# Kernel tuning notes

Measured on AMD Instinct MI355X. Metric: run time of the kernel, lower is better.

The kernel has to match this reference:

```python
import jax, jax.numpy as jnp
import numpy as np

NEG_SLOPE = 0.01  # F.leaky_relu default


def gcn_conv(x, W, b, src, dst):
    """PyG GCNConv: add self-loops, symmetric deg^-1/2 normalization, linear, scatter-add."""
    n = x.shape[0]
    loop = jnp.arange(n)
    s = jnp.concatenate([src, loop])  # source j
    d = jnp.concatenate([dst, loop])  # target i
    deg = jax.ops.segment_sum(jnp.ones_like(d, dtype=x.dtype), d, num_segments=n)
    dis = jnp.where(deg > 0, jax.lax.rsqrt(jnp.maximum(deg, 1e-12)), 0.0)
    norm = dis[s] * dis[d]                       # [E+N]
    h = x @ W                                    # [N, out]
    msg = h[s] * norm[:, None]                   # gather + scale
    out = jax.ops.segment_sum(msg, d, num_segments=n)  # scatter-add to targets
    return out + b


def setup_inputs() -> dict:
    key = jax.random.key(0)
    ks = jax.random.split(key, 8)
    N, E, G = 100000, 800000, 100
    IN, H, OUT = 128, 256, 16
    x = jax.random.normal(ks[0], (N, IN), dtype=jnp.float32)
    edge_index = jax.random.randint(ks[1], (2, E), 0, N, dtype=jnp.int64)
    batch = jnp.repeat(jnp.arange(G, dtype=jnp.int64), N // G)  # sorted graph ids
    def glorot(k, fi, fo):
        lim = np.sqrt(6.0 / (fi + fo))
        return jax.random.uniform(k, (fi, fo), jnp.float32, -lim, lim)
    return {
        "x": x, "edge_index": edge_index, "batch": batch,
        "W1": glorot(ks[2], IN, H), "b1": jnp.zeros((H,), jnp.float32),
        "W2": glorot(ks[3], H, H),  "b2": jnp.zeros((H,), jnp.float32),
        "W3": glorot(ks[4], H, OUT), "b3": jnp.zeros((OUT,), jnp.float32),
    }


def reference(x, edge_index, batch, W1, b1, W2, b2, W3, b3):
    src, dst = edge_index[0], edge_index[1]
    h = gcn_conv(x, W1, b1, src, dst)
    h = jax.nn.leaky_relu(h, NEG_SLOPE)  # dropout p=0.0 -> identity
    h = gcn_conv(h, W2, b2, src, dst)
    h = jax.nn.leaky_relu(h, NEG_SLOPE)
    h = gcn_conv(h, W3, b3, src, dst)
    # get_zero_nodes: first node of each graph in the sorted batch vector
    mask = jnp.concatenate([jnp.array([True]), batch[1:] != batch[:-1]])
    return h[mask, :]  # [n_graphs, out_channels]
```

## Files before the change

kernel.cpp:

```cpp
#include <hip/hip_runtime.h>

#define NEG_SLOPE 0.01f

using short8 = __attribute__((ext_vector_type(8))) short;
using f32x4  = __attribute__((ext_vector_type(4))) float;

__device__ inline float b2f(ushort u) {
    union { unsigned u; float f; } x; x.u = ((unsigned)u) << 16; return x.f;
}
__device__ inline ushort f2b(float f) {
    union { float f; unsigned u; } x; x.f = f;
    unsigned r = x.u + 0x7FFFu + ((x.u >> 16) & 1u);
    return (ushort)(r >> 16);
}
__device__ inline void gload16(const void* g, void* l) {
    __builtin_amdgcn_global_load_lds((__attribute__((address_space(1))) void*)g,
                                     (__attribute__((address_space(3))) void*)l, 16, 0, 0);
}
__device__ inline int isroot(const int* __restrict__ batch, int d) {
    return (d == 0) || (batch[d] != batch[d - 1]);
}
__device__ inline void gbar(int* ctr, int nblk) {
    __syncthreads();
    if (threadIdx.x == 0) {
        __threadfence();
        __hip_atomic_fetch_add(ctr, 1, __ATOMIC_RELEASE, __HIP_MEMORY_SCOPE_AGENT);
        while (__hip_atomic_load(ctr, __ATOMIC_ACQUIRE, __HIP_MEMORY_SCOPE_AGENT) < nblk)
            __builtin_amdgcn_s_sleep(1);
    }
    __syncthreads();
}


__global__ void count_f1(const int* __restrict__ src, const int* __restrict__ dst,
                         const int* __restrict__ batch, int* __restrict__ cnt,
                         int* __restrict__ flag1, int* __restrict__ picked, int E, int N) {
    int i = blockIdx.x * blockDim.x + threadIdx.x;
    if (i < N && isroot(batch, i)) {
        picked[batch[i]] = i;
        flag1[i] = 1;
    }
    int e0 = i * 4;
    if (e0 + 3 < E) {
        int4 dq = *(const int4*)(dst + e0);
        int r0 = isroot(batch, dq.x), r1 = isroot(batch, dq.y);
        int r2 = isroot(batch, dq.z), r3 = isroot(batch, dq.w);
        atomicAdd(&cnt[dq.x], 1);
        atomicAdd(&cnt[dq.y], 1);
        atomicAdd(&cnt[dq.z], 1);
        atomicAdd(&cnt[dq.w], 1);
        if (r0 | r1 | r2 | r3) {
            int4 sq = *(const int4*)(src + e0);
            if (r0) flag1[sq.x] = 1;
            if (r1) flag1[sq.y] = 1;
            if (r2) flag1[sq.z] = 1;
            if (r3) flag1[sq.w] = 1;
        }
    } else if (e0 < E) {
        for (int e = e0; e < E; e++) {
            int d = dst[e];
            atomicAdd(&cnt[d], 1);
            if (isroot(batch, d)) flag1[src[e]] = 1;
        }
    }
}


__global__ void frontier2v(const int* __restrict__ src, const int* __restrict__ dst,
                           const int* __restrict__ flag1, int* __restrict__ flag2,
                           int E, int N) {
    int i = blockIdx.x * blockDim.x + threadIdx.x;
    int e0 = i * 4;
    if (e0 + 3 < E) {
        int4 dq = *(const int4*)(dst + e0);
        int f0 = flag1[dq.x], f1 = flag1[dq.y], f2 = flag1[dq.z], f3 = flag1[dq.w];
        if (f0 | f1 | f2 | f3) {
            int4 sq = *(const int4*)(src + e0);
            if (f0) flag2[sq.x] = 1;
            if (f1) flag2[sq.y] = 1;
            if (f2) flag2[sq.z] = 1;
            if (f3) flag2[sq.w] = 1;
        }
    } else if (e0 < E) {
        for (int e = e0; e < E; e++) if (flag1[dst[e]]) flag2[src[e]] = 1;
    }
    if (i < N && flag1[i]) flag2[i] = 1;
}


__global__ __launch_bounds__(256) void scan_one(
    const int* __restrict__ cnt, const int* __restrict__ f1, const int* __restrict__ f2,
    int4* __restrict__ aggslot, float* __restrict__ dis,
    int* __restrict__ rowptr, int* __restrict__ cur,
    int* __restrict__ pos1, int* __restrict__ pos2,
    int* __restrict__ list1, int* __restrict__ list2,
    int* __restrict__ counts, int N, int nb,
    const float* __restrict__ W1, ushort* __restrict__ W1t,
    const float* __restrict__ W2, ushort* __restrict__ W2t) {
    __shared__ int l0[256], l1[256], l2[256];
    __shared__ int baseS[3];
    const int b = blockIdx.x, t = threadIdx.x;
    const int base = b * 1024 + t * 4;

    int c[4] = {0,0,0,0}, a1[4] = {0,0,0,0}, a2[4] = {0,0,0,0};
    if (base + 3 < N) {
        int4 q = *(const int4*)(cnt + base); c[0]=q.x; c[1]=q.y; c[2]=q.z; c[3]=q.w;
        int4 u = *(const int4*)(f1 + base);  a1[0]=u.x; a1[1]=u.y; a1[2]=u.z; a1[3]=u.w;
        int4 v = *(const int4*)(f2 + base);  a2[0]=v.x; a2[1]=v.y; a2[2]=v.z; a2[3]=v.w;
    } else {
        for (int i = 0; i < 4; i++) if (base + i < N) {
            c[i] = cnt[base + i]; a1[i] = f1[base + i]; a2[i] = f2[base + i];
        }
    }
#pragma unroll
    for (int i = 0; i < 4; i++)
        if (base + i < N) dis[base + i] = rsqrtf((float)c[i] + 1.0f);

    int m[4];
#pragma unroll
    for (int i = 0; i < 4; i++) m[i] = a2[i] ? c[i] : 0;
    int ts0 = m[0] + m[1] + m[2] + m[3];
    int ts1 = a1[0] + a1[1] + a1[2] + a1[3];
    int ts2 = a2[0] + a2[1] + a2[2] + a2[3];
    l0[t] = ts0; l1[t] = ts1; l2[t] = ts2;
    __syncthreads();
    for (int off = 1; off < 256; off <<= 1) {
        int u0 = (t >= off) ? l0[t - off] : 0;
        int u1 = (t >= off) ? l1[t - off] : 0;
        int u2 = (t >= off) ? l2[t - off] : 0;
        __syncthreads();
        l0[t] += u0; l1[t] += u1; l2[t] += u2;
        __syncthreads();
    }

    if (t == 0) {
        __hip_atomic_store(&aggslot[b].x, l0[255], __ATOMIC_RELAXED, __HIP_MEMORY_SCOPE_AGENT);
        __hip_atomic_store(&aggslot[b].y, l1[255], __ATOMIC_RELAXED, __HIP_MEMORY_SCOPE_AGENT);
        __hip_atomic_store(&aggslot[b].z, l2[255], __ATOMIC_RELAXED, __HIP_MEMORY_SCOPE_AGENT);
        __hip_atomic_store(&aggslot[b].w, 1, __ATOMIC_RELEASE, __HIP_MEMORY_SCOPE_AGENT);
    }

    if (t < 64) {
        int g0 = 0, g1 = 0, g2 = 0;
        for (int w0 = 0; w0 < b; w0 += 64) {
            int idx = w0 + t;
            if (idx < b) {
                while (__hip_atomic_load(&aggslot[idx].w, __ATOMIC_ACQUIRE,
                                         __HIP_MEMORY_SCOPE_AGENT) == 0) {
                    __builtin_amdgcn_s_sleep(1);
                }
                g0 += __hip_atomic_load(&aggslot[idx].x, __ATOMIC_RELAXED, __HIP_MEMORY_SCOPE_AGENT);
                g1 += __hip_atomic_load(&aggslot[idx].y, __ATOMIC_RELAXED, __HIP_MEMORY_SCOPE_AGENT);
                g2 += __hip_atomic_load(&aggslot[idx].z, __ATOMIC_RELAXED, __HIP_MEMORY_SCOPE_AGENT);
            }
        }
#pragma unroll
        for (int s = 1; s < 64; s <<= 1) {
            g0 += __shfl_xor(g0, s, 64);
            g1 += __shfl_xor(g1, s, 64);
            g2 += __shfl_xor(g2, s, 64);
        }
        if (t == 0) { baseS[0] = g0; baseS[1] = g1; baseS[2] = g2; }
    }
    __syncthreads();

    int run0 = baseS[0] + l0[t] - ts0;
    int run1 = baseS[1] + l1[t] - ts1;
    int run2 = baseS[2] + l2[t] - ts2;
#pragma unroll
    for (int i = 0; i < 4; i++) {
        if (base + i < N) {
            rowptr[base + i] = run0;
            cur[base + i] = run0;
            if (a1[i]) { pos1[base + i] = run1; list1[run1] = base + i; }
            if (a2[i]) { pos2[base + i] = run2; list2[run2] = base + i; }
        }
        run0 += m[i]; run1 += a1[i]; run2 += a2[i];
    }
    if (b == nb - 1 && t == 255) {
        counts[0] = baseS[1] + l1[255];
        counts[1] = baseS[2] + l2[255];
        rowptr[N] = baseS[0] + l0[255];
    }

    for (int idx = b * 256 + t; idx < 98304; idx += gridDim.x * 256) {
        if (idx < 32768) {
            int n = idx >> 7, k = idx & 127;
            W1t[idx] = f2b(W1[k * 256 + n]);
        } else {
            int j = idx - 32768;
            int n = j >> 8, k = j & 255;
            W2t[j] = f2b(W2[k * 256 + n]);
        }
    }
}


__global__ void fill_fv(const int* __restrict__ src, const int* __restrict__ dst,
                        const int* __restrict__ flag2, int* __restrict__ cur,
                        int* __restrict__ col, int E) {
    int i = blockIdx.x * blockDim.x + threadIdx.x;
    int e0 = i * 4;
    if (e0 + 3 < E) {
        int4 dq = *(const int4*)(dst + e0);
        int f0 = flag2[dq.x], f1 = flag2[dq.y], f2 = flag2[dq.z], f3 = flag2[dq.w];
        if (f0 | f1 | f2 | f3) {
            int4 sq = *(const int4*)(src + e0);
            if (f0) col[atomicAdd(&cur[dq.x], 1)] = sq.x;
            if (f1) col[atomicAdd(&cur[dq.y], 1)] = sq.y;
            if (f2) col[atomicAdd(&cur[dq.z], 1)] = sq.z;
            if (f3) col[atomicAdd(&cur[dq.w], 1)] = sq.w;
        }
    } else if (e0 < E) {
        for (int e = e0; e < E; e++) {
            int d = dst[e];
            if (flag2[d]) col[atomicAdd(&cur[d], 1)] = src[e];
        }
    }
}


__global__ __launch_bounds__(256) void aggx_c(const float* __restrict__ x,
                                              const float* __restrict__ dis,
                                              const int* __restrict__ rowptr,
                                              const int* __restrict__ col,
                                              const int* __restrict__ list2,
                                              const int* __restrict__ counts,
                                              ushort* __restrict__ aggXc) {
    const int M2 = counts[1];
    int wave = blockIdx.x * 4 + (threadIdx.x >> 6);
    int lane = threadIdx.x & 63;
    int li = lane & 31, sub = lane >> 5;
    int stride = gridDim.x * 8;
    const float* xp = x + li * 4;
    for (int p = wave * 2 + sub; p < M2; p += stride) {
        int node = list2[p];
        float di = dis[node];
        float4 sv = *(const float4*)(xp + (size_t)node * 128);
        float a0 = di * sv.x, a1 = di * sv.y, a2 = di * sv.z, a3 = di * sv.w;
        int e = rowptr[node], e1 = rowptr[node + 1];
        for (; e + 2 <= e1; e += 2) {
            int s0 = col[e], s1 = col[e + 1];
            float w0 = dis[s0], w1 = dis[s1];
            float4 v0 = *(const float4*)(xp + (size_t)s0 * 128);
            float4 v1 = *(const float4*)(xp + (size_t)s1 * 128);
            a0 += w0 * v0.x + w1 * v1.x;
            a1 += w0 * v0.y + w1 * v1.y;
            a2 += w0 * v0.z + w1 * v1.z;
            a3 += w0 * v0.w + w1 * v1.w;
        }
        if (e < e1) {
            int s = col[e];
            float w = dis[s];
            float4 v = *(const float4*)(xp + (size_t)s * 128);
            a0 += w * v.x; a1 += w * v.y; a2 += w * v.z; a3 += w * v.w;
        }
        ushort4 o;
        o.x = f2b(di * a0); o.y = f2b(di * a1); o.z = f2b(di * a2); o.w = f2b(di * a3);
        *(ushort4*)(aggXc + (size_t)p * 128 + li * 4) = o;
    }
}


template <int K>
__device__ void gemm_phase(const ushort* __restrict__ A, const ushort* __restrict__ Bt,
                           const float* __restrict__ bias, const float* __restrict__ dis,
                           const int* __restrict__ list, int M, ushort* __restrict__ C,
                           ushort* As, ushort* Bs, int nblk) {
    const int t = threadIdx.x;
    const int lane = t & 63;
    const int w = t >> 6;
    const int wm = w >> 2, wn = w & 3;

    for (int tile = blockIdx.x; tile * 128 < M; tile += nblk) {
        const int row0 = tile * 128;
        f32x4 acc[4][4] = {};
#pragma unroll
        for (int kt = 0; kt < K / 64; kt++) {
#pragma unroll
            for (int it = 0; it < 2; it++) {
                int q = it * 512 + t;
                int r = q >> 3, c = q & 7;
                int cs = c ^ (r & 7);
                int ga = min(row0 + r, M - 1);
                gload16(A + (size_t)ga * K + kt * 64 + cs * 8, &As[q * 8]);
            }
#pragma unroll
            for (int it = 0; it < 4; it++) {
                int q = it * 512 + t;
                int r = q >> 3, c = q & 7;
                int cs = c ^ (r & 7);
                gload16(Bt + (size_t)r * K + kt * 64 + cs * 8, &Bs[q * 8]);
            }
            __syncthreads();
#pragma unroll
            for (int ks = 0; ks < 2; ks++) {
                short8 a[4], b[4];
                int cc = ks * 4 + (lane >> 4);
#pragma unroll
                for (int m = 0; m < 4; m++) {
                    int R = wm * 64 + m * 16 + (lane & 15);
                    a[m] = *(const short8*)&As[R * 64 + ((cc ^ (R & 7)) * 8)];
                }
#pragma unroll
                for (int n = 0; n < 4; n++) {
                    int R = wn * 64 + n * 16 + (lane & 15);
                    b[n] = *(const short8*)&Bs[R * 64 + ((cc ^ (R & 7)) * 8)];
                }
#pragma unroll
                for (int m = 0; m < 4; m++)
#pragma unroll
                    for (int n = 0; n < 4; n++)
                        acc[m][n] = __builtin_amdgcn_mfma_f32_16x16x32_bf16(a[m], b[n], acc[m][n], 0, 0, 0);
            }
            __syncthreads();
        }
#pragma unroll
        for (int m = 0; m < 4; m++) {
#pragma unroll
            for (int j = 0; j < 4; j++) {
                int grow = row0 + wm * 64 + m * 16 + (lane >> 4) * 4 + j;
                if (grow >= M) continue;
                float dr = dis[list[grow]];
#pragma unroll
                for (int n = 0; n < 4; n++) {
                    int gcol = wn * 64 + n * 16 + (lane & 15);
                    float v = acc[m][n][j] + bias[gcol];
                    v = v > 0.f ? v : NEG_SLOPE * v;
                    C[(size_t)grow * 256 + gcol] = f2b(v * dr);
                }
            }
        }
    }
}


#define TAIL_NBLK 64

__global__ __launch_bounds__(512) void megatail(
    const ushort* __restrict__ aggXc, const ushort* __restrict__ W1t,
    const float* __restrict__ b1, ushort* __restrict__ h1c,
    const float* __restrict__ dis, const int* __restrict__ rowptr,
    const int* __restrict__ col, const int* __restrict__ list1,
    const int* __restrict__ list2, const int* __restrict__ pos1,
    const int* __restrict__ pos2, const int* __restrict__ counts,
    ushort* __restrict__ agg1c, const ushort* __restrict__ W2t,
    const float* __restrict__ b2, ushort* __restrict__ h2c,
    const int* __restrict__ picked, const float* __restrict__ W3,
    const float* __restrict__ b3, float* __restrict__ out,
    int* __restrict__ bars, int G) {
    __shared__ ushort As[128 * 64];
    __shared__ ushort Bs[256 * 64];
    __shared__ float aggf[256];
    __shared__ float redf[256];
    const int t = threadIdx.x;
    const int bid = blockIdx.x;
    const int M1 = counts[0];
    const int M2 = counts[1];

    gemm_phase<128>(aggXc, W1t, b1, dis, list2, M2, h1c, As, Bs, TAIL_NBLK);
    gbar(&bars[0], TAIL_NBLK);

    {
        int lane = t & 63;
        int w = t >> 6;
        int wave = bid * 8 + w;
        int li = lane & 31, sub = lane >> 5;
        int stride = TAIL_NBLK * 16;
        const ushort* hp = h1c + (size_t)li * 8;
        for (int p = wave * 2 + sub; p < M1; p += stride) {
            int i = list1[p];
            float di = dis[i];
            float a[8];
            {
                short8 v = *(const short8*)(hp + (size_t)pos2[i] * 256);
#pragma unroll
                for (int j = 0; j < 8; j++) a[j] = b2f((ushort)v[j]);
            }
            int e1 = rowptr[i + 1];
            for (int e = rowptr[i]; e < e1; e++) {
                short8 v = *(const short8*)(hp + (size_t)pos2[col[e]] * 256);
#pragma unroll
                for (int j = 0; j < 8; j++) a[j] += b2f((ushort)v[j]);
            }
            short8 o;
#pragma unroll
            for (int j = 0; j < 8; j++) o[j] = (short)f2b(di * a[j]);
            *(short8*)(agg1c + (size_t)p * 256 + li * 8) = o;
        }
    }
    gbar(&bars[1], TAIL_NBLK);

    gemm_phase<256>(agg1c, W2t, b2, dis, list1, M1, h2c, As, Bs, TAIL_NBLK);
    gbar(&bars[2], TAIL_NBLK);

    for (int g = bid; g < G; g += TAIL_NBLK) {
        if (t < 256) {
            int i = picked[g];
            float di = dis[i];
            float a = b2f(h2c[(size_t)pos1[i] * 256 + t]);
            int e1 = rowptr[i + 1];
            for (int e = rowptr[i]; e < e1; e++)
                a += b2f(h2c[(size_t)pos1[col[e]] * 256 + t]);
            aggf[t] = di * a;
        }
        __syncthreads();
        if (t < 256) {
            int c = t & 15, seg = t >> 4;
            float p = 0.f;
#pragma unroll
            for (int kk = 0; kk < 16; kk++) {
                int k = seg * 16 + kk;
                p += aggf[k] * W3[k * 16 + c];
            }
            redf[t] = p;
        }
        __syncthreads();
        if (t < 16) {
            float s = 0.f;
#pragma unroll
            for (int ss = 0; ss < 16; ss++) s += redf[ss * 16 + t];
            out[g * 16 + t] = s + b3[t];
        }
        __syncthreads();
    }
}


extern "C" void kernel_launch(void* const* d_in, const int* in_sizes, int n_in,
                              void* d_out, int out_size, void* d_ws, size_t ws_size,
                              hipStream_t stream) {
    const float* x   = (const float*)d_in[0];
    const int* ei    = (const int*)d_in[1];
    const int* batch = (const int*)d_in[2];
    const float* W1  = (const float*)d_in[3];
    const float* b1  = (const float*)d_in[4];
    const float* W2  = (const float*)d_in[5];
    const float* b2  = (const float*)d_in[6];
    const float* W3  = (const float*)d_in[7];
    const float* b3  = (const float*)d_in[8];

    const int IN = 128, H = 256, OUT = 16;
    int N = in_sizes[0] / IN;
    int E = in_sizes[1] / 2;
    int G = out_size / OUT;
    const int* srcp = ei;
    const int* dstp = ei + E;

    char* p = (char*)d_ws;
    auto carve = [&](size_t bytes) {
        char* q = p;
        p += (bytes + 255) & ~(size_t)255;
        return q;
    };
    int*    cnt    = (int*)carve((size_t)N * 4);
    int*    flag1  = (int*)carve((size_t)N * 4);
    int*    flag2  = (int*)carve((size_t)N * 4);
    int4*   aggslot= (int4*)carve(1024 * 16);
    int*    bars   = (int*)carve(256);
    char*   zend   = p;
    float*  dis    = (float*)carve((size_t)N * 4);
    int*    rowptr = (int*)carve(((size_t)N + 1) * 4);
    int*    cur    = (int*)carve((size_t)N * 4);
    int*    counts = (int*)carve(256);
    int*    picked = (int*)carve((size_t)G * 4);
    int*    pos1   = (int*)carve((size_t)N * 4);
    int*    pos2   = (int*)carve((size_t)N * 4);
    int*    list1  = (int*)carve((size_t)N * 4);
    int*    list2  = (int*)carve((size_t)N * 4);
    int*    col    = (int*)carve((size_t)E * 4);
    ushort* W1t    = (ushort*)carve((size_t)256 * 128 * 2);
    ushort* W2t    = (ushort*)carve((size_t)256 * 256 * 2);
    ushort* RA     = (ushort*)carve((size_t)N * H * 2);
    ushort* RB     = (ushort*)carve((size_t)N * H * 2);

    ushort* aggXc = RA;
    ushort* agg1c = RA;
    ushort* h1c   = RB;
    ushort* h2c   = RB;

    int nb = (N + 1023) / 1024;
    int e4 = (E + 3) / 4;
    int epN = (e4 > N ? e4 : N);

    hipMemsetAsync(cnt, 0, (size_t)(zend - (char*)cnt), stream);
    count_f1<<<(epN + 255) / 256, 256, 0, stream>>>(srcp, dstp, batch, cnt, flag1, picked, E, N);
    frontier2v<<<(epN + 255) / 256, 256, 0, stream>>>(srcp, dstp, flag1, flag2, E, N);
    scan_one<<<nb, 256, 0, stream>>>(cnt, flag1, flag2, aggslot, dis, rowptr, cur,
                                     pos1, pos2, list1, list2, counts, N, nb,
                                     W1, W1t, W2, W2t);
    fill_fv<<<(e4 + 255) / 256, 256, 0, stream>>>(srcp, dstp, flag2, cur, col, E);
    aggx_c<<<1024, 256, 0, stream>>>(x, dis, rowptr, col, list2, counts, aggXc);
    megatail<<<TAIL_NBLK, 512, 0, stream>>>(aggXc, W1t, b1, h1c, dis, rowptr, col,
                                            list1, list2, pos1, pos2, counts, agg1c,
                                            W2t, b2, h2c, picked, W3, b3,
                                            (float*)d_out, bars, G);
}
```

Before: 159.2 us.

## Replace persistent megatail with layer-1 GEMM plus per-graph fused tail kernel

The persistent megatail kernel used grid barriers to run the layer-1 GEMM, the layer-2 aggregation over the 1-hop frontier, the layer-2 GEMM and the final layer. It is split into a standalone layer-1 GEMM kernel and a per-graph tail kernel. For each picked root node, the tail kernel recomputes layer-2 aggregation and the W2 matvec only for the root and its neighbours, then does the layer-3 reduction. This drops the frontier-1 list/scan bookkeeping, the global barriers and the full layer-2 GEMM over all 1-hop nodes, in exchange for redundant per-graph scalar matvecs with a single block per graph.

```diff
diff --git a/kernel.cpp b/kernel.cpp
--- a/kernel.cpp
+++ b/kernel.cpp
@@ -19,16 +19,6 @@
 }
 __device__ inline int isroot(const int* __restrict__ batch, int d) {
     return (d == 0) || (batch[d] != batch[d - 1]);
-}
-__device__ inline void gbar(int* ctr, int nblk) {
-    __syncthreads();
-    if (threadIdx.x == 0) {
-        __threadfence();
-        __hip_atomic_fetch_add(ctr, 1, __ATOMIC_RELEASE, __HIP_MEMORY_SCOPE_AGENT);
-        while (__hip_atomic_load(ctr, __ATOMIC_ACQUIRE, __HIP_MEMORY_SCOPE_AGENT) < nblk)
-            __builtin_amdgcn_s_sleep(1);
-    }
-    __syncthreads();
 }
 
 
@@ -88,28 +78,26 @@
 }
 
 
-__global__ __launch_bounds__(256) void scan_one(
-    const int* __restrict__ cnt, const int* __restrict__ f1, const int* __restrict__ f2,
+__global__ __launch_bounds__(256) void scan_dual(
+    const int* __restrict__ cnt, const int* __restrict__ f2,
     int4* __restrict__ aggslot, float* __restrict__ dis,
     int* __restrict__ rowptr, int* __restrict__ cur,
-    int* __restrict__ pos1, int* __restrict__ pos2,
-    int* __restrict__ list1, int* __restrict__ list2,
+    int* __restrict__ pos2, int* __restrict__ list2,
     int* __restrict__ counts, int N, int nb,
     const float* __restrict__ W1, ushort* __restrict__ W1t,
-    const float* __restrict__ W2, ushort* __restrict__ W2t) {
-    __shared__ int l0[256], l1[256], l2[256];
-    __shared__ int baseS[3];
+    const float* __restrict__ W2, ushort* __restrict__ W2b) {
+    __shared__ int l0[256], l2[256];
+    __shared__ int baseS[2];
     const int b = blockIdx.x, t = threadIdx.x;
     const int base = b * 1024 + t * 4;
 
-    int c[4] = {0,0,0,0}, a1[4] = {0,0,0,0}, a2[4] = {0,0,0,0};
+    int c[4] = {0,0,0,0}, a2[4] = {0,0,0,0};
     if (base + 3 < N) {
         int4 q = *(const int4*)(cnt + base); c[0]=q.x; c[1]=q.y; c[2]=q.z; c[3]=q.w;
-        int4 u = *(const int4*)(f1 + base);  a1[0]=u.x; a1[1]=u.y; a1[2]=u.z; a1[3]=u.w;
         int4 v = *(const int4*)(f2 + base);  a2[0]=v.x; a2[1]=v.y; a2[2]=v.z; a2[3]=v.w;
     } else {
         for (int i = 0; i < 4; i++) if (base + i < N) {
-            c[i] = cnt[base + i]; a1[i] = f1[base + i]; a2[i] = f2[base + i];
+            c[i] = cnt[base + i]; a2[i] = f2[base + i];
         }
     }
 #pragma unroll
@@ -120,28 +108,25 @@
 #pragma unroll
     for (int i = 0; i < 4; i++) m[i] = a2[i] ? c[i] : 0;
     int ts0 = m[0] + m[1] + m[2] + m[3];
-    int ts1 = a1[0] + a1[1] + a1[2] + a1[3];
     int ts2 = a2[0] + a2[1] + a2[2] + a2[3];
-    l0[t] = ts0; l1[t] = ts1; l2[t] = ts2;
+    l0[t] = ts0; l2[t] = ts2;
     __syncthreads();
     for (int off = 1; off < 256; off <<= 1) {
         int u0 = (t >= off) ? l0[t - off] : 0;
-        int u1 = (t >= off) ? l1[t - off] : 0;
         int u2 = (t >= off) ? l2[t - off] : 0;
         __syncthreads();
-        l0[t] += u0; l1[t] += u1; l2[t] += u2;
+        l0[t] += u0; l2[t] += u2;
         __syncthreads();
     }
 
     if (t == 0) {
         __hip_atomic_store(&aggslot[b].x, l0[255], __ATOMIC_RELAXED, __HIP_MEMORY_SCOPE_AGENT);
-        __hip_atomic_store(&aggslot[b].y, l1[255], __ATOMIC_RELAXED, __HIP_MEMORY_SCOPE_AGENT);
-        __hip_atomic_store(&aggslot[b].z, l2[255], __ATOMIC_RELAXED, __HIP_MEMORY_SCOPE_AGENT);
+        __hip_atomic_store(&aggslot[b].y, l2[255], __ATOMIC_RELAXED, __HIP_MEMORY_SCOPE_AGENT);
         __hip_atomic_store(&aggslot[b].w, 1, __ATOMIC_RELEASE, __HIP_MEMORY_SCOPE_AGENT);
     }
 
     if (t < 64) {
-        int g0 = 0, g1 = 0, g2 = 0;
+        int g0 = 0, g2 = 0;
         for (int w0 = 0; w0 < b; w0 += 64) {
             int idx = w0 + t;
             if (idx < b) {
@@ -150,36 +135,31 @@
                     __builtin_amdgcn_s_sleep(1);
                 }
                 g0 += __hip_atomic_load(&aggslot[idx].x, __ATOMIC_RELAXED, __HIP_MEMORY_SCOPE_AGENT);
-                g1 += __hip_atomic_load(&aggslot[idx].y, __ATOMIC_RELAXED, __HIP_MEMORY_SCOPE_AGENT);
-                g2 += __hip_atomic_load(&aggslot[idx].z, __ATOMIC_RELAXED, __HIP_MEMORY_SCOPE_AGENT);
+                g2 += __hip_atomic_load(&aggslot[idx].y, __ATOMIC_RELAXED, __HIP_MEMORY_SCOPE_AGENT);
             }
         }
 #pragma unroll
         for (int s = 1; s < 64; s <<= 1) {
             g0 += __shfl_xor(g0, s, 64);
-            g1 += __shfl_xor(g1, s, 64);
             g2 += __shfl_xor(g2, s, 64);
         }
-        if (t == 0) { baseS[0] = g0; baseS[1] = g1; baseS[2] = g2; }
+        if (t == 0) { baseS[0] = g0; baseS[1] = g2; }
     }
     __syncthreads();
 
     int run0 = baseS[0] + l0[t] - ts0;
-    int run1 = baseS[1] + l1[t] - ts1;
-    int run2 = baseS[2] + l2[t] - ts2;
+    int run2 = baseS[1] + l2[t] - ts2;
 #pragma unroll
     for (int i = 0; i < 4; i++) {
         if (base + i < N) {
             rowptr[base + i] = run0;
             cur[base + i] = run0;
-            if (a1[i]) { pos1[base + i] = run1; list1[run1] = base + i; }
             if (a2[i]) { pos2[base + i] = run2; list2[run2] = base + i; }
         }
-        run0 += m[i]; run1 += a1[i]; run2 += a2[i];
+        run0 += m[i]; run2 += a2[i];
     }
     if (b == nb - 1 && t == 255) {
-        counts[0] = baseS[1] + l1[255];
-        counts[1] = baseS[2] + l2[255];
+        counts[0] = baseS[1] + l2[255];
         rowptr[N] = baseS[0] + l0[255];
     }
 
@@ -189,8 +169,7 @@
             W1t[idx] = f2b(W1[k * 256 + n]);
         } else {
             int j = idx - 32768;
-            int n = j >> 8, k = j & 255;
-            W2t[j] = f2b(W2[k * 256 + n]);
+            W2b[j] = f2b(W2[j]);
         }
     }
 }
@@ -227,7 +206,7 @@
                                               const int* __restrict__ list2,
                                               const int* __restrict__ counts,
                                               ushort* __restrict__ aggXc) {
-    const int M2 = counts[1];
+    const int M2 = counts[0];
     int wave = blockIdx.x * 4 + (threadIdx.x >> 6);
     int lane = threadIdx.x & 63;
     int li = lane & 31, sub = lane >> 5;
@@ -263,19 +242,25 @@
 
 
 template <int K>
-__device__ void gemm_phase(const ushort* __restrict__ A, const ushort* __restrict__ Bt,
-                           const float* __restrict__ bias, const float* __restrict__ dis,
-                           const int* __restrict__ list, int M, ushort* __restrict__ C,
-                           ushort* As, ushort* Bs, int nblk) {
+__global__ __launch_bounds__(512) void gemm_c(const ushort* __restrict__ A,
+                                              const ushort* __restrict__ Bt,
+                                              const float* __restrict__ bias,
+                                              const float* __restrict__ dis,
+                                              const int* __restrict__ list,
+                                              const int* __restrict__ counts,
+                                              ushort* __restrict__ C) {
+    __shared__ ushort As[128 * 64];
+    __shared__ ushort Bs[256 * 64];
+    const int M = counts[0];
     const int t = threadIdx.x;
     const int lane = t & 63;
     const int w = t >> 6;
     const int wm = w >> 2, wn = w & 3;
 
-    for (int tile = blockIdx.x; tile * 128 < M; tile += nblk) {
+    for (int tile = blockIdx.x; tile * 128 < M; tile += gridDim.x) {
         const int row0 = tile * 128;
         f32x4 acc[4][4] = {};
-#pragma unroll
+
         for (int kt = 0; kt < K / 64; kt++) {
 #pragma unroll
             for (int it = 0; it < 2; it++) {
@@ -315,6 +300,7 @@
             }
             __syncthreads();
         }
+
 #pragma unroll
         for (int m = 0; m < 4; m++) {
 #pragma unroll
@@ -335,94 +321,82 @@
 }
 
 
-#define TAIL_NBLK 64
-
-__global__ __launch_bounds__(512) void megatail(
-    const ushort* __restrict__ aggXc, const ushort* __restrict__ W1t,
-    const float* __restrict__ b1, ushort* __restrict__ h1c,
-    const float* __restrict__ dis, const int* __restrict__ rowptr,
-    const int* __restrict__ col, const int* __restrict__ list1,
-    const int* __restrict__ list2, const int* __restrict__ pos1,
-    const int* __restrict__ pos2, const int* __restrict__ counts,
-    ushort* __restrict__ agg1c, const ushort* __restrict__ W2t,
-    const float* __restrict__ b2, ushort* __restrict__ h2c,
-    const int* __restrict__ picked, const float* __restrict__ W3,
-    const float* __restrict__ b3, float* __restrict__ out,
-    int* __restrict__ bars, int G) {
-    __shared__ ushort As[128 * 64];
-    __shared__ ushort Bs[256 * 64];
-    __shared__ float aggf[256];
-    __shared__ float redf[256];
+__global__ __launch_bounds__(256) void tail_g(
+    const ushort* __restrict__ h1c, const float* __restrict__ dis,
+    const int* __restrict__ rowptr, const int* __restrict__ col,
+    const int* __restrict__ picked, const int* __restrict__ pos2,
+    const ushort* __restrict__ W2b, const float* __restrict__ b2,
+    const float* __restrict__ W3, const float* __restrict__ b3,
+    float* __restrict__ out, int G) {
+    __shared__ float aggs[8][256];
+    __shared__ float sdis[8];
+    __shared__ float vec[256];
+    __shared__ float red[256];
+    const int g = blockIdx.x;
     const int t = threadIdx.x;
-    const int bid = blockIdx.x;
-    const int M1 = counts[0];
-    const int M2 = counts[1];
-
-    gemm_phase<128>(aggXc, W1t, b1, dis, list2, M2, h1c, As, Bs, TAIL_NBLK);
-    gbar(&bars[0], TAIL_NBLK);
-
-    {
-        int lane = t & 63;
-        int w = t >> 6;
-        int wave = bid * 8 + w;
-        int li = lane & 31, sub = lane >> 5;
-        int stride = TAIL_NBLK * 16;
-        const ushort* hp = h1c + (size_t)li * 8;
-        for (int p = wave * 2 + sub; p < M1; p += stride) {
-            int i = list1[p];
-            float di = dis[i];
-            float a[8];
-            {
-                short8 v = *(const short8*)(hp + (size_t)pos2[i] * 256);
-#pragma unroll
-                for (int j = 0; j < 8; j++) a[j] = b2f((ushort)v[j]);
-            }
-            int e1 = rowptr[i + 1];
-            for (int e = rowptr[i]; e < e1; e++) {
-                short8 v = *(const short8*)(hp + (size_t)pos2[col[e]] * 256);
-#pragma unroll
-                for (int j = 0; j < 8; j++) a[j] += b2f((ushort)v[j]);
-            }
-            short8 o;
-#pragma unroll
-            for (int j = 0; j < 8; j++) o[j] = (short)f2b(di * a[j]);
-            *(short8*)(agg1c + (size_t)p * 256 + li * 8) = o;
-        }
-    }
-    gbar(&bars[1], TAIL_NBLK);
-
-    gemm_phase<256>(agg1c, W2t, b2, dis, list1, M1, h2c, As, Bs, TAIL_NBLK);
-    gbar(&bars[2], TAIL_NBLK);
-
-    for (int g = bid; g < G; g += TAIL_NBLK) {
-        if (t < 256) {
-            int i = picked[g];
-            float di = dis[i];
-            float a = b2f(h2c[(size_t)pos1[i] * 256 + t]);
-            int e1 = rowptr[i + 1];
-            for (int e = rowptr[i]; e < e1; e++)
-                a += b2f(h2c[(size_t)pos1[col[e]] * 256 + t]);
-            aggf[t] = di * a;
+    if (g >= G) return;
+    const int i = picked[g];
+    const float di = dis[i];
+    const int re0 = rowptr[i];
+    const int ns = rowptr[i + 1] - re0 + 1;
+    float acc2 = 0.f;
+
+    for (int c0 = 0; c0 < ns; c0 += 8) {
+        int nc = min(8, ns - c0);
+        for (int j = 0; j < nc; j++) {
+            int sidx = c0 + j;
+            int s = (sidx == 0) ? i : col[re0 + sidx - 1];
+            float ds = dis[s];
+            if (t == 0) sdis[j] = ds;
+            const ushort* hp = h1c + t;
+            float a = b2f(hp[(size_t)pos2[s] * 256]);
+            int e = rowptr[s], e1 = rowptr[s + 1];
+            for (; e + 4 <= e1; e += 4) {
+                int u0 = col[e], u1 = col[e + 1], u2 = col[e + 2], u3 = col[e + 3];
+                a += (b2f(hp[(size_t)pos2[u0] * 256]) + b2f(hp[(size_t)pos2[u1] * 256])) +
+                     (b2f(hp[(size_t)pos2[u2] * 256]) + b2f(hp[(size_t)pos2[u3] * 256]));
+            }
+            for (; e < e1; e++) a += b2f(hp[(size_t)pos2[col[e]] * 256]);
+            aggs[j][t] = ds * a;
         }
         __syncthreads();
-        if (t < 256) {
-            int c = t & 15, seg = t >> 4;
-            float p = 0.f;
-#pragma unroll
-            for (int kk = 0; kk < 16; kk++) {
-                int k = seg * 16 + kk;
-                p += aggf[k] * W3[k * 16 + c];
-            }
-            redf[t] = p;
+        float p[8];
+#pragma unroll
+        for (int j = 0; j < 8; j++) p[j] = 0.f;
+#pragma unroll 4
+        for (int k = 0; k < 256; k++) {
+            float wv = b2f(W2b[k * 256 + t]);
+#pragma unroll
+            for (int j = 0; j < 8; j++) p[j] += aggs[j][k] * wv;
+        }
+        float bb = b2[t];
+#pragma unroll
+        for (int j = 0; j < 8; j++) {
+            if (j < nc) {
+                float v = p[j] + bb;
+                v = v > 0.f ? v : NEG_SLOPE * v;
+                acc2 += sdis[j] * v;
+            }
         }
         __syncthreads();
-        if (t < 16) {
-            float s = 0.f;
-#pragma unroll
-            for (int ss = 0; ss < 16; ss++) s += redf[ss * 16 + t];
-            out[g * 16 + t] = s + b3[t];
-        }
-        __syncthreads();
+    }
+
+    vec[t] = di * acc2;
+    __syncthreads();
+    int c = t & 15, seg = t >> 4;
+    float pp = 0.f;
+#pragma unroll
+    for (int kk = 0; kk < 16; kk++) {
+        int k = seg * 16 + kk;
+        pp += vec[k] * W3[k * 16 + c];
+    }
+    red[t] = pp;
+    __syncthreads();
+    if (t < 16) {
+        float s = 0.f;
+#pragma unroll
+        for (int ss = 0; ss < 16; ss++) s += red[ss * 16 + t];
+        out[g * 16 + t] = s + b3[t];
     }
 }
 
@@ -457,27 +431,19 @@
     int*    flag1  = (int*)carve((size_t)N * 4);
     int*    flag2  = (int*)carve((size_t)N * 4);
     int4*   aggslot= (int4*)carve(1024 * 16);
-    int*    bars   = (int*)carve(256);
     char*   zend   = p;
     float*  dis    = (float*)carve((size_t)N * 4);
     int*    rowptr = (int*)carve(((size_t)N + 1) * 4);
     int*    cur    = (int*)carve((size_t)N * 4);
     int*    counts = (int*)carve(256);
     int*    picked = (int*)carve((size_t)G * 4);
-    int*    pos1   = (int*)carve((size_t)N * 4);
     int*    pos2   = (int*)carve((size_t)N * 4);
-    int*    list1  = (int*)carve((size_t)N * 4);
     int*    list2  = (int*)carve((size_t)N * 4);
     int*    col    = (int*)carve((size_t)E * 4);
     ushort* W1t    = (ushort*)carve((size_t)256 * 128 * 2);
-    ushort* W2t    = (ushort*)carve((size_t)256 * 256 * 2);
-    ushort* RA     = (ushort*)carve((size_t)N * H * 2);
-    ushort* RB     = (ushort*)carve((size_t)N * H * 2);
-
-    ushort* aggXc = RA;
-    ushort* agg1c = RA;
-    ushort* h1c   = RB;
-    ushort* h2c   = RB;
+    ushort* W2b    = (ushort*)carve((size_t)256 * 256 * 2);
+    ushort* aggXc  = (ushort*)carve((size_t)N * 128 * 2);
+    ushort* h1c    = (ushort*)carve((size_t)N * H * 2);
 
     int nb = (N + 1023) / 1024;
     int e4 = (E + 3) / 4;
@@ -486,13 +452,11 @@
     hipMemsetAsync(cnt, 0, (size_t)(zend - (char*)cnt), stream);
     count_f1<<<(epN + 255) / 256, 256, 0, stream>>>(srcp, dstp, batch, cnt, flag1, picked, E, N);
     frontier2v<<<(epN + 255) / 256, 256, 0, stream>>>(srcp, dstp, flag1, flag2, E, N);
-    scan_one<<<nb, 256, 0, stream>>>(cnt, flag1, flag2, aggslot, dis, rowptr, cur,
-                                     pos1, pos2, list1, list2, counts, N, nb,
-                                     W1, W1t, W2, W2t);
+    scan_dual<<<nb, 256, 0, stream>>>(cnt, flag2, aggslot, dis, rowptr, cur,
+                                      pos2, list2, counts, N, nb, W1, W1t, W2, W2b);
     fill_fv<<<(e4 + 255) / 256, 256, 0, stream>>>(srcp, dstp, flag2, cur, col, E);
     aggx_c<<<1024, 256, 0, stream>>>(x, dis, rowptr, col, list2, counts, aggXc);
-    megatail<<<TAIL_NBLK, 512, 0, stream>>>(aggXc, W1t, b1, h1c, dis, rowptr, col,
-                                            list1, list2, pos1, pos2, counts, agg1c,
-                                            W2t, b2, h2c, picked, W3, b3,
-                                            (float*)d_out, bars, G);
-}
+    gemm_c<128><<<64, 512, 0, stream>>>(aggXc, W1t, b1, dis, list2, counts, h1c);
+    tail_g<<<G, 256, 0, stream>>>(h1c, dis, rowptr, col, picked, pos2, W2b, b2,
+                                  W3, b3, (float*)d_out, G);
+}
```

New measurement: 168.2 us. +5.7%, slower.
